# Performance work log

Measured on AMD Instinct MI355X. Metric: run time of the kernel, lower is better.

Reference implementation:

```python
import jax, jax.numpy as jnp
import numpy as np

EPS = 1e-5

def _ln(x, g, b):
    m = jnp.mean(x, axis=-1, keepdims=True)
    v = jnp.var(x, axis=-1, keepdims=True)
    return (x - m) / jnp.sqrt(v + EPS) * g + b

def _partition(x, nw):
    b, h, w, c = x.shape
    x = x.reshape(b, nw, h // nw, nw, w // nw, c).transpose(0, 1, 3, 2, 4, 5)
    return x.reshape(b * nw * nw, h // nw, w // nw, c)

def _merge(x, nw):
    b_, h, w, c = x.shape
    b = b_ // (nw * nw)
    x = x.reshape(b, nw, nw, h, w, c).transpose(0, 1, 3, 2, 4, 5)
    return x.reshape(b, nw * h, nw * w, c)

def _window_attn(q, k, v, width, height, nw, mask):
    b, _, c = q.shape
    q = q.reshape(b, height, width, c)
    k = k.reshape(b, height, width, c)
    v = v.reshape(b, height, width, c)
    sh, sw = (height // nw) // 2, (width // nw) // 2
    q = jnp.roll(q, (-sh, -sw), (1, 2))
    k = jnp.roll(k, (-sh, -sw), (1, 2))
    v = jnp.roll(v, (-sh, -sw), (1, 2))
    q = _partition(q, nw); k = _partition(k, nw); v = _partition(v, nw)
    N = (height // nw) * (width // nw)
    b_ = b * nw * nw
    qf = q.reshape(b_, N, c); kf = k.reshape(b_, N, c); vf = v.reshape(b_, N, c)
    scale = jnp.asarray(c, qf.dtype) ** 0.5
    scores = jnp.einsum('bnc,bmc->bnm', qf, kf) / scale  # [b_, N, N]
    scores = (scores.reshape(b, nw * nw, N, N) + mask[None]).reshape(b_, N, N)
    attn = jax.nn.softmax(scores, axis=-1)
    out = jnp.einsum('bnm,bmc->bnc', attn, vf)
    out = _merge(out.reshape(b_, height // nw, width // nw, c), nw)
    out = jnp.roll(out, (sh, sw), (1, 2))
    return out.reshape(b, height * width, c)

def _block(feat0, feat1, width, height, mask, nw, wq, wk, wv, wfc, g, be, ffn=None):
    q = feat0 @ wq; k = feat1 @ wk; v = feat1 @ wv
    a = _window_attn(q, k, v, width, height, nw, mask)
    a = _ln(a @ wfc, g, be)
    if ffn is not None:
        w1, w2, fg, fb = ffn
        h = jax.nn.gelu(jnp.concatenate([feat0, a], axis=-1) @ w1, approximate=False)
        a = _ln(h @ w2, fg, fb)
    return feat0 + a

def setup_inputs() -> dict:
    key = jax.random.key(0)
    B, H, W, NW, D = 8, 128, 128, 8, 256
    N = (H // NW) * (W // NW)
    ks = jax.random.split(key, 16)
    s = D ** -0.5
    return {
        'feat0': jax.random.normal(ks[0], (B, H * W, D), jnp.float32),
        'feat1': jax.random.normal(ks[1], (B, H * W, D), jnp.float32),
        'mask_attn': jax.random.normal(ks[2], (NW * NW, N, N), jnp.float32),
        'width': W, 'height': H, 'n_window': NW,
        'intra_wq': jax.random.normal(ks[3], (D, D), jnp.float32) * s,
        'intra_wk': jax.random.normal(ks[4], (D, D), jnp.float32) * s,
        'intra_wv': jax.random.normal(ks[5], (D, D), jnp.float32) * s,
        'intra_wfc': jax.random.normal(ks[6], (D, D), jnp.float32) * s,
        'intra_g': jnp.ones((D,), jnp.float32),
        'intra_b': jnp.zeros((D,), jnp.float32),
        'inter_wq': jax.random.normal(ks[7], (D, D), jnp.float32) * s,
        'inter_wk': jax.random.normal(ks[8], (D, D), jnp.float32) * s,
        'inter_wv': jax.random.normal(ks[9], (D, D), jnp.float32) * s,
        'inter_wfc': jax.random.normal(ks[10], (D, D), jnp.float32) * s,
        'inter_g': jnp.ones((D,), jnp.float32),
        'inter_b': jnp.zeros((D,), jnp.float32),
        'inter_w1': jax.random.normal(ks[11], (2 * D, 2 * D * 4), jnp.float32) * (2 * D) ** -0.5,
        'inter_w2': jax.random.normal(ks[12], (2 * D * 4, D), jnp.float32) * (2 * D * 4) ** -0.5,
        'inter_fg': jnp.ones((D,), jnp.float32),
        'inter_fb': jnp.zeros((D,), jnp.float32),
    }

def reference(feat0, feat1, mask_attn, width, height, n_window,
              intra_wq, intra_wk, intra_wv, intra_wfc, intra_g, intra_b,
              inter_wq, inter_wk, inter_wv, inter_wfc, inter_g, inter_b,
              inter_w1, inter_w2, inter_fg, inter_fb):
    f0 = _block(feat0, feat0, width, height, mask_attn, n_window,
                intra_wq, intra_wk, intra_wv, intra_wfc, intra_g, intra_b)
    out = _block(f0, feat1, width, height, mask_attn, n_window,
                 inter_wq, inter_wk, inter_wv, inter_wfc, inter_g, inter_b,
                 ffn=(inter_w1, inter_w2, inter_fg, inter_fb))
    return out
```

## Files before the change

### kernel.cpp

```cpp
#include <hip/hip_runtime.h>

typedef unsigned short u16;
typedef unsigned int   u32;

using f32x4  = __attribute__((ext_vector_type(4))) float;
using bf16x8 = __attribute__((ext_vector_type(8))) __bf16;

__device__ inline u16 f2bf(float f) {
  return __builtin_bit_cast(u16, (__bf16)f);
}
__device__ inline float bf2f(u16 v) {
  u32 u = ((u32)v) << 16;
  return __builtin_bit_cast(float, u);
}
__device__ inline u32 pk_bf16(float a, float b) {
  u32 d;
  asm("v_cvt_pk_bf16_f32 %0, %1, %2" : "=v"(d) : "v"(a), "v"(b));
  return d;
}

__device__ inline void gl_lds16(const u16* g, u16* l) {
  __builtin_amdgcn_global_load_lds((const __attribute__((address_space(1))) void*)g,
                                   (__attribute__((address_space(3))) void*)l,
                                   16, 0, 0);
}

__device__ inline int perm_fwd(int m) {
  int b = m >> 14, rem = m & 16383;
  int h = rem >> 7, w = rem & 127;
  int hr = (h - 8) & 127, wr = (w - 8) & 127;
  int win = (b << 6) | ((hr >> 4) << 3) | (wr >> 4);
  return (win << 8) | ((hr & 15) << 4) | (wr & 15);
}
__device__ inline int perm_inv(int r) {
  int win = r >> 8, t = r & 255;
  int b = win >> 6, wy = (win >> 3) & 7, wx = win & 7;
  int h = (((wy << 4) | (t >> 4)) + 8) & 127;
  int w = (((wx << 4) | (t & 15)) + 8) & 127;
  return (b << 14) | (h << 7) | w;
}


enum { MODE_QKV = 0, MODE_PV = 2, MODE_FFN1 = 4 };

template<int MODE>
__global__ __launch_bounds__(256)
void gemm_nt(const u16* __restrict__ A, int lda, long long sAz,
             const u16* __restrict__ Bt, int ldb, long long sBz,
             u16* __restrict__ OutB, float* __restrict__ OutF,
             const float* __restrict__ mask, int K, int ldo)
{
  __shared__ __align__(16) u16 sA[128 * 64];
  __shared__ __align__(16) u16 sB[128 * 64];

  const int tid  = threadIdx.x;
  const int lane = tid & 63;
  const int wave = tid >> 6;
  const int l15  = lane & 15;
  const int quad = lane >> 4;
  const int wm   = (wave >> 1) << 6;
  const int wn   = (wave & 1) << 6;
  const int z    = blockIdx.z;
  const int m0   = (int)(blockIdx.y) << 7;
  const int n0   = (int)(blockIdx.x) << 7;

  const u16* Ab = A  + (long long)z * sAz;
  const u16* Bb = Bt + (long long)z * sBz;

  const int cd = ((lane & 7) ^ ((lane >> 3) & 7)) << 3;
  const int rs = (wave << 5) + (lane >> 3);
  const u16* ga0 = Ab + (long long)(m0 + rs) * lda + cd;
  const u16* gb0 = Bb + (long long)(n0 + rs) * ldb + cd;
  u16* la0 = &sA[wave << 11];
  u16* lb0 = &sB[wave << 11];

  const f32x4 zero = {0.f, 0.f, 0.f, 0.f};
  f32x4 acc[4][4];
#pragma unroll
  for (int i = 0; i < 4; ++i)
#pragma unroll
    for (int j = 0; j < 4; ++j) acc[i][j] = zero;

  for (int k0 = 0; k0 < K; k0 += 64) {
    __syncthreads();
#pragma unroll
    for (int p = 0; p < 4; ++p) {
      gl_lds16(ga0 + k0 + (p << 3) * lda, la0 + (p << 9));
      gl_lds16(gb0 + k0 + (p << 3) * ldb, lb0 + (p << 9));
    }
    __syncthreads();
#pragma unroll
    for (int kk = 0; kk < 2; ++kk) {
      const int sw = (((quad | (kk << 2)) ^ (l15 & 7)) << 3);
      bf16x8 af[4], bfr[4];
#pragma unroll
      for (int i = 0; i < 4; ++i) {
        af[i]  = *(const bf16x8*)(sA + ((wm + (i << 4) + l15) << 6) + sw);
        bfr[i] = *(const bf16x8*)(sB + ((wn + (i << 4) + l15) << 6) + sw);
      }
#pragma unroll
      for (int i = 0; i < 4; ++i)
#pragma unroll
        for (int j = 0; j < 4; ++j)
          acc[i][j] = __builtin_amdgcn_mfma_f32_16x16x32_bf16(af[i], bfr[j], acc[i][j], 0, 0, 0);
    }
  }

#pragma unroll
  for (int i = 0; i < 4; ++i) {
#pragma unroll
    for (int r = 0; r < 4; ++r) {
      int mg = m0 + wm + (i << 4) + (quad << 2) + r;
      if constexpr (MODE == MODE_QKV) {
        u16* orow = OutB + (long long)(n0 >> 8) * ldo + ((long long)perm_fwd(mg) << 8);
#pragma unroll
        for (int j = 0; j < 4; ++j) {
          int ng = n0 + wn + (j << 4) + l15;
          orow[ng & 255] = f2bf(acc[i][j][r]);
        }
      } else if constexpr (MODE == MODE_PV) {
        u16* orow = OutB + ((long long)perm_inv((z << 8) + mg) << 8);
#pragma unroll
        for (int j = 0; j < 4; ++j) {
          int ng = n0 + wn + (j << 4) + l15;
          orow[ng] = f2bf(acc[i][j][r]);
        }
      } else {
        float gv[4];
#pragma unroll
        for (int j = 0; j < 4; ++j) {
          float v = acc[i][j][r];
          float t = v * fmaf(v * v, -0.071354816f, -1.5957691216f);
          gv[j] = v * __builtin_amdgcn_rcpf(1.0f + __expf(t));
        }
        uint2 d;
        d.x = pk_bf16(gv[0], gv[1]);
        d.y = pk_bf16(gv[2], gv[3]);
        *(uint2*)(OutB + (long long)mg * ldo + n0 + wn + (l15 << 2)) = d;
      }
    }
  }
}

__global__ __launch_bounds__(256)
void gemm_vt(const u16* __restrict__ Wt,
             const u16* __restrict__ Feat,
             u16* __restrict__ Vt)
{
  __shared__ __align__(16) u16 sA[128 * 64];
  __shared__ __align__(16) u16 sB[128 * 64];

  const int tid  = threadIdx.x;
  const int lane = tid & 63;
  const int wave = tid >> 6;
  const int l15  = lane & 15;
  const int quad = lane >> 4;
  const int wm   = (wave >> 1) << 6;
  const int wn   = (wave & 1) << 6;
  const int z    = blockIdx.z;
  const int m0   = (int)(blockIdx.y) << 7;
  const int n0   = (int)(blockIdx.x) << 7;

  const int cd = ((lane & 7) ^ ((lane >> 3) & 7)) << 3;
  const int rs = (wave << 5) + (lane >> 3);
  const u16* ga0 = Wt + (long long)(m0 + rs) * 256 + cd;
  const u16* gb0 = Feat + (long long)perm_inv((z << 8) + n0 + rs)        * 256 + cd;
  const u16* gb1 = Feat + (long long)perm_inv((z << 8) + n0 + rs + 8)    * 256 + cd;
  const u16* gb2 = Feat + (long long)perm_inv((z << 8) + n0 + rs + 16)   * 256 + cd;
  const u16* gb3 = Feat + (long long)perm_inv((z << 8) + n0 + rs + 24)   * 256 + cd;
  u16* la0 = &sA[wave << 11];
  u16* lb0 = &sB[wave << 11];

  const f32x4 zero = {0.f, 0.f, 0.f, 0.f};
  f32x4 acc[4][4];
#pragma unroll
  for (int i = 0; i < 4; ++i)
#pragma unroll
    for (int j = 0; j < 4; ++j) acc[i][j] = zero;

  for (int k0 = 0; k0 < 256; k0 += 64) {
    __syncthreads();
#pragma unroll
    for (int p = 0; p < 4; ++p)
      gl_lds16(ga0 + k0 + (p << 3) * 256, la0 + (p << 9));
    gl_lds16(gb0 + k0, lb0);
    gl_lds16(gb1 + k0, lb0 + 512);
    gl_lds16(gb2 + k0, lb0 + 1024);
    gl_lds16(gb3 + k0, lb0 + 1536);
    __syncthreads();
#pragma unroll
    for (int kk = 0; kk < 2; ++kk) {
      const int sw = (((quad | (kk << 2)) ^ (l15 & 7)) << 3);
      bf16x8 af[4], bfr[4];
#pragma unroll
      for (int i = 0; i < 4; ++i) {
        af[i]  = *(const bf16x8*)(sA + ((wm + (i << 4) + l15) << 6) + sw);
        bfr[i] = *(const bf16x8*)(sB + ((wn + (i << 4) + l15) << 6) + sw);
      }
#pragma unroll
      for (int i = 0; i < 4; ++i)
#pragma unroll
        for (int j = 0; j < 4; ++j)
          acc[i][j] = __builtin_amdgcn_mfma_f32_16x16x32_bf16(af[i], bfr[j], acc[i][j], 0, 0, 0);
    }
  }

#pragma unroll
  for (int i = 0; i < 4; ++i) {
#pragma unroll
    for (int r = 0; r < 4; ++r) {
      const int mg = m0 + wm + (i << 4) + (quad << 2) + r;
      u16* orow = Vt + (((long long)z) << 16) + ((long long)mg << 8);
#pragma unroll
      for (int j = 0; j < 4; ++j) {
        int ng = n0 + wn + (j << 4) + l15;
        orow[ng] = f2bf(acc[i][j][r]);
      }
    }
  }
}

__global__ __launch_bounds__(256)
void scores_softmax(const u16* __restrict__ Q, const u16* __restrict__ Kw,
                    const float* __restrict__ mask, u16* __restrict__ SP)
{
  __shared__ __align__(16) u16 sA[128 * 64];
  __shared__ __align__(16) u16 sB[256 * 64];

  const int tid  = threadIdx.x;
  const int lane = tid & 63;
  const int wave = tid >> 6;
  const int l15  = lane & 15;
  const int quad = lane >> 4;

  const int mhalf = (int)blockIdx.x;
  const int z     = (int)blockIdx.y;
  const int m0    = mhalf << 7;

  const u16* Ab = Q  + ((long long)z << 16);
  const u16* Bb = Kw + ((long long)z << 16);

  const int cd  = ((lane & 7) ^ ((lane >> 3) & 7)) << 3;
  const int rsA = (wave << 5) + (lane >> 3);
  const int rsB = (wave << 6) + (lane >> 3);
  const u16* ga0 = Ab + (long long)(m0 + rsA) * 256 + cd;
  const u16* gb0 = Bb + (long long)rsB * 256 + cd;
  u16* la0 = &sA[wave << 11];
  u16* lb0 = &sB[wave << 12];

  const f32x4 zero = {0.f, 0.f, 0.f, 0.f};
  f32x4 acc[2][16];
#pragma unroll
  for (int i = 0; i < 2; ++i)
#pragma unroll
    for (int j = 0; j < 16; ++j) acc[i][j] = zero;

  for (int k0 = 0; k0 < 256; k0 += 64) {
    __syncthreads();
#pragma unroll
    for (int p = 0; p < 4; ++p)
      gl_lds16(ga0 + k0 + (p << 3) * 256, la0 + (p << 9));
#pragma unroll
    for (int p = 0; p < 8; ++p)
      gl_lds16(gb0 + k0 + (p << 3) * 256, lb0 + (p << 9));
    __syncthreads();
#pragma unroll
    for (int kk = 0; kk < 2; ++kk) {
      const int sw = (((quad | (kk << 2)) ^ (l15 & 7)) << 3);
      bf16x8 af0 = *(const bf16x8*)(sA + (((wave << 5) + l15) << 6) + sw);
      bf16x8 af1 = *(const bf16x8*)(sA + (((wave << 5) + 16 + l15) << 6) + sw);
#pragma unroll
      for (int j = 0; j < 16; ++j) {
        bf16x8 bf = *(const bf16x8*)(sB + (((j << 4) + l15) << 6) + sw);
        acc[0][j] = __builtin_amdgcn_mfma_f32_16x16x32_bf16(af0, bf, acc[0][j], 0, 0, 0);
        acc[1][j] = __builtin_amdgcn_mfma_f32_16x16x32_bf16(af1, bf, acc[1][j], 0, 0, 0);
      }
    }
  }

  const float* mbase = mask + (((long long)(z & 63)) << 16);
#pragma unroll
  for (int i = 0; i < 2; ++i) {
#pragma unroll
    for (int r = 0; r < 4; ++r) {
      const int mg = m0 + (wave << 5) + (i << 4) + (quad << 2) + r;
      const float* mrow = mbase + ((long long)mg << 8);
      float sv[16];
      float mx = -3.0e38f;
#pragma unroll
      for (int j = 0; j < 16; ++j) {
        sv[j] = acc[i][j][r] * 0.0625f + mrow[(j << 4) + l15];
        mx = fmaxf(mx, sv[j]);
      }
#pragma unroll
      for (int o = 1; o < 16; o <<= 1) mx = fmaxf(mx, __shfl_xor(mx, o));
      float sum = 0.f;
#pragma unroll
      for (int j = 0; j < 16; ++j) { sv[j] = __expf(sv[j] - mx); sum += sv[j]; }
#pragma unroll
      for (int o = 1; o < 16; o <<= 1) sum += __shfl_xor(sum, o);
      const float inv = 1.0f / sum;
      u16* orow = SP + (((long long)z) << 16) + ((long long)mg << 8);
#pragma unroll
      for (int j = 0; j < 16; ++j) orow[(j << 4) + l15] = f2bf(sv[j] * inv);
    }
  }
}

enum { LN_XCAT0 = 0, LN_XCAT1 = 1, LN_OUT = 2 };

template<int MODE>
__global__ __launch_bounds__(256)
void gemm_ln(const u16* __restrict__ A, int lda,
             const u16* __restrict__ Bt,
             const float* __restrict__ G, const float* __restrict__ Bias,
             const float* __restrict__ ResF, const u16* __restrict__ ResB,
             float* __restrict__ OutF, u16* __restrict__ OutB, int K)
{
  __shared__ __align__(16) u16 sA[64 * 64];
  __shared__ __align__(16) u16 sB[256 * 64];

  const int tid  = threadIdx.x;
  const int lane = tid & 63;
  const int wave = tid >> 6;
  const int l15  = lane & 15;
  const int quad = lane >> 4;
  const int m0   = (int)blockIdx.x << 6;

  const int cd  = ((lane & 7) ^ ((lane >> 3) & 7)) << 3;
  const int rsA = (wave << 4) + (lane >> 3);
  const int rsB = (wave << 6) + (lane >> 3);
  const u16* ga0 = A  + (long long)(m0 + rsA) * lda + cd;
  const u16* gb0 = Bt + (long long)rsB * K + cd;
  u16* la0 = &sA[wave << 10];
  u16* lb0 = &sB[wave << 12];

  const f32x4 zero = {0.f, 0.f, 0.f, 0.f};
  f32x4 acc[16];
#pragma unroll
  for (int j = 0; j < 16; ++j) acc[j] = zero;

  for (int k0 = 0; k0 < K; k0 += 64) {
    __syncthreads();
#pragma unroll
    for (int p = 0; p < 2; ++p)
      gl_lds16(ga0 + k0 + (p << 3) * lda, la0 + (p << 9));
#pragma unroll
    for (int p = 0; p < 8; ++p)
      gl_lds16(gb0 + k0 + (p << 3) * K, lb0 + (p << 9));
    __syncthreads();
#pragma unroll
    for (int kk = 0; kk < 2; ++kk) {
      const int sw = (((quad | (kk << 2)) ^ (l15 & 7)) << 3);
      bf16x8 af = *(const bf16x8*)(sA + (((wave << 4) + l15) << 6) + sw);
#pragma unroll
      for (int j = 0; j < 16; ++j) {
        bf16x8 bf = *(const bf16x8*)(sB + (((j << 4) + l15) << 6) + sw);
        acc[j] = __builtin_amdgcn_mfma_f32_16x16x32_bf16(af, bf, acc[j], 0, 0, 0);
      }
    }
  }

  float gj[16], bj[16];
#pragma unroll
  for (int j = 0; j < 16; ++j) {
    gj[j] = G[(j << 4) + l15];
    bj[j] = Bias[(j << 4) + l15];
  }

#pragma unroll
  for (int r = 0; r < 4; ++r) {
    const int mg = m0 + (wave << 4) + (quad << 2) + r;
    float s = 0.f, s2 = 0.f;
#pragma unroll
    for (int j = 0; j < 16; ++j) {
      float v = acc[j][r];
      s += v; s2 += v * v;
    }
#pragma unroll
    for (int o = 1; o < 16; o <<= 1) { s += __shfl_xor(s, o); s2 += __shfl_xor(s2, o); }
    const float mean = s * (1.0f / 256.0f);
    const float var  = s2 * (1.0f / 256.0f) - mean * mean;
    const float rstd = rsqrtf(var + 1e-5f);
    if constexpr (MODE == LN_XCAT0) {
      u16* orow = OutB + ((long long)mg << 9);
      const float* rrow = ResF + ((long long)mg << 8);
#pragma unroll
      for (int j = 0; j < 16; ++j) {
        float v = (acc[j][r] - mean) * rstd * gj[j] + bj[j];
        orow[(j << 4) + l15] = f2bf(v + rrow[(j << 4) + l15]);
      }
    } else if constexpr (MODE == LN_XCAT1) {
      u16* orow = OutB + ((long long)mg << 9) + 256;
#pragma unroll
      for (int j = 0; j < 16; ++j) {
        float v = (acc[j][r] - mean) * rstd * gj[j] + bj[j];
        orow[(j << 4) + l15] = f2bf(v);
      }
    } else {
      const u16* rrow = ResB + ((long long)mg << 9);
      float* orow = OutF + ((long long)mg << 8);
#pragma unroll
      for (int j = 0; j < 16; ++j) {
        float v = (acc[j][r] - mean) * rstd * gj[j] + bj[j];
        orow[(j << 4) + l15] = v + bf2f(rrow[(j << 4) + l15]);
      }
    }
  }
}

__global__ __launch_bounds__(256)
void cvt_f32_bf16(const float* __restrict__ src, u16* __restrict__ dst, int n4)
{
  int i = blockIdx.x * 256 + threadIdx.x;
  if (i >= n4) return;
  float4 v = ((const float4*)src)[i];
  ushort4 u; u.x = f2bf(v.x); u.y = f2bf(v.y); u.z = f2bf(v.z); u.w = f2bf(v.w);
  ((ushort4*)dst)[i] = u;
}

__global__ __launch_bounds__(256)
void wtrans(const float* __restrict__ src, u16* __restrict__ dst, int R, int C)
{
  int idx = blockIdx.x * 256 + threadIdx.x;
  if (idx >= R * C) return;
  int r = idx / C, c = idx - r * C;
  dst[c * R + r] = f2bf(src[idx]);
}

__global__ __launch_bounds__(256)
void wtrans_w2(const float* __restrict__ src, u16* __restrict__ dst)
{
  int idx = blockIdx.x * 256 + threadIdx.x;
  int c = idx >> 11, q = idx & 2047;
  int f = (q & ~63) | ((q & 3) << 4) | ((q >> 2) & 15);
  dst[idx] = f2bf(src[f * 256 + c]);
}

extern "C" void kernel_launch(void* const* d_in, const int* in_sizes, int n_in,
                              void* d_out, int out_size, void* d_ws, size_t ws_size,
                              hipStream_t stream)
{
  (void)in_sizes; (void)n_in; (void)out_size;
  const float* feat0 = (const float*)d_in[0];
  const float* feat1 = (const float*)d_in[1];
  const float* mask  = (const float*)d_in[2];
  const float* wq1 = (const float*)d_in[6];
  const float* wk1 = (const float*)d_in[7];
  const float* wv1 = (const float*)d_in[8];
  const float* wf1 = (const float*)d_in[9];
  const float* g1  = (const float*)d_in[10];
  const float* b1  = (const float*)d_in[11];
  const float* wq2 = (const float*)d_in[12];
  const float* wk2 = (const float*)d_in[13];
  const float* wv2 = (const float*)d_in[14];
  const float* wf2 = (const float*)d_in[15];
  const float* g2  = (const float*)d_in[16];
  const float* b2  = (const float*)d_in[17];
  const float* w1  = (const float*)d_in[18];
  const float* w2  = (const float*)d_in[19];
  const float* fg  = (const float*)d_in[20];
  const float* fb  = (const float*)d_in[21];

  const size_t Mi = 1048576;
  const size_t WB = 4 * Mi;
  const int Mtot = 131072;

  int nc = 8;
  for (int c = 1; c <= 8; c <<= 1) {
    size_t S = (size_t)(Mtot / c) * 512;
    if (7 * S + WB <= ws_size) { nc = c; break; }
  }
  const int Mc = Mtot / nc;
  const size_t S = (size_t)Mc * 512;

  char* ws = (char*)d_ws;
  u16*   featb = (u16*)(ws);
  u16*   SPb   = featb;
  u16*   qw    = (u16*)(ws + S);
  u16*   Ob    = qw;
  u16*   hbuf  = featb;
  u16*   kw    = (u16*)(ws + 2 * S);
  u16*   vt    = (u16*)(ws + 4 * S);
  u16*   xcat  = (u16*)(ws + 5 * S);
  u16*   wb    = (u16*)(ws + 7 * S);
  u16* wq1t = wb;            u16* wk1t = wb + 65536;  u16* wv1t = wb + 131072; u16* wf1t = wb + 196608;
  u16* wq2t = wb + 262144;   u16* wk2t = wb + 327680; u16* wv2t = wb + 393216; u16* wf2t = wb + 458752;
  u16* w1t  = wb + 524288;
  u16* w2t  = wb + 524288 + 1048576;

  const dim3 blk(256);
  const dim3 gBig(2, Mc / 128, 1);
  const dim3 gQK(4, Mc / 128, 1);
  const int  Wc = Mc / 256;
  const dim3 gWin(2, 2, Wc);
  const dim3 gSS(2, Wc);
  const int  gRows = Mc / 4;
  const int  gLN   = Mc / 64;
  const int  MF = Mc / 2;
  const dim3 gF1(16, MF / 128, 1);
  const int  gLNF  = MF / 64;

  wtrans<<<256, blk, 0, stream>>>(wq1, wq1t, 256, 256);
  wtrans<<<256, blk, 0, stream>>>(wk1, wk1t, 256, 256);
  wtrans<<<256, blk, 0, stream>>>(wv1, wv1t, 256, 256);
  wtrans<<<256, blk, 0, stream>>>(wf1, wf1t, 256, 256);
  wtrans<<<256, blk, 0, stream>>>(wq2, wq2t, 256, 256);
  wtrans<<<256, blk, 0, stream>>>(wk2, wk2t, 256, 256);
  wtrans<<<256, blk, 0, stream>>>(wv2, wv2t, 256, 256);
  wtrans<<<256, blk, 0, stream>>>(wf2, wf2t, 256, 256);
  wtrans<<<4096, blk, 0, stream>>>(w1, w1t, 512, 2048);
  wtrans_w2<<<2048, blk, 0, stream>>>(w2, w2t);

  const int qkStride = Mc * 256;

  for (int c = 0; c < nc; ++c) {
    const long long off = (long long)c * Mc * 256;
    const float* f0in = feat0 + off;
    const float* f1in = feat1 + off;
    float* outp = (float*)d_out + off;

    cvt_f32_bf16<<<gRows, blk, 0, stream>>>(f0in, featb, Mc * 64);
    gemm_nt<MODE_QKV><<<gQK, blk, 0, stream>>>(featb, 256, 0, wq1t, 256, 0, qw, nullptr, nullptr, 256, qkStride);
    gemm_vt<<<gWin, blk, 0, stream>>>(wv1t, featb, vt);
    scores_softmax<<<gSS, blk, 0, stream>>>(qw, kw, mask, SPb);
    gemm_nt<MODE_PV><<<gWin, blk, 0, stream>>>(SPb, 256, 65536, vt, 256, 65536, Ob, nullptr, nullptr, 256, 0);
    gemm_ln<LN_XCAT0><<<gLN, blk, 0, stream>>>(Ob, 256, wf1t, g1, b1, f0in, nullptr, nullptr, xcat, 256);

    cvt_f32_bf16<<<gRows, blk, 0, stream>>>(f1in, featb, Mc * 64);
    gemm_nt<MODE_QKV><<<gBig, blk, 0, stream>>>(xcat, 512, 0, wq2t, 256, 0, qw, nullptr, nullptr, 512, 0);
    gemm_nt<MODE_QKV><<<gBig, blk, 0, stream>>>(featb, 256, 0, wk2t, 256, 0, kw, nullptr, nullptr, 256, 0);
    gemm_vt<<<gWin, blk, 0, stream>>>(wv2t, featb, vt);
    scores_softmax<<<gSS, blk, 0, stream>>>(qw, kw, mask, SPb);
    gemm_nt<MODE_PV><<<gWin, blk, 0, stream>>>(SPb, 256, 65536, vt, 256, 65536, Ob, nullptr, nullptr, 256, 0);
    gemm_ln<LN_XCAT1><<<gLN, blk, 0, stream>>>(Ob, 256, wf2t, g2, b2, nullptr, nullptr, nullptr, xcat, 256);

    for (int mc = 0; mc < 2; ++mc) {
      const u16* xc = xcat + (long long)mc * MF * 512;
      gemm_nt<MODE_FFN1><<<gF1, blk, 0, stream>>>(xc, 512, 0, w1t, 512, 0,
                                                  hbuf, nullptr, nullptr, 512, 2048);
      gemm_ln<LN_OUT><<<gLNF, blk, 0, stream>>>(hbuf, 2048, w2t, fg, fb, nullptr,
                                                xcat + (long long)mc * MF * 512,
                                                outp + (long long)mc * MF * 256, nullptr, 2048);
    }
  }
}
```

Baseline: 1.664 ms.

## Double-buffer LDS tiles with K=32 steps to overlap global loads with MFMA

All four GEMM-style kernels move from a single 64-wide K tile to two 32-wide LDS buffers. The next tile is prefetched via global_load_lds while MFMAs run on the current one, and each iteration needs one barrier instead of two. The LDS swizzle and row mapping are reworked for the 32-element row width. In exchange the loop has twice as many iterations, and the prefetch relies on the end-of-loop barrier to make the async LDS writes visible. That barrier may not wait for the outstanding global-load-to-LDS traffic unless the compiler inserts a vmcnt wait.

```diff
diff --git a/kernel.cpp b/kernel.cpp
--- a/kernel.cpp
+++ b/kernel.cpp
@@ -50,8 +50,8 @@
              u16* __restrict__ OutB, float* __restrict__ OutF,
              const float* __restrict__ mask, int K, int ldo)
 {
-  __shared__ __align__(16) u16 sA[128 * 64];
-  __shared__ __align__(16) u16 sB[128 * 64];
+  __shared__ __align__(16) u16 sA[2][128 * 32];
+  __shared__ __align__(16) u16 sB[2][128 * 32];
 
   const int tid  = threadIdx.x;
   const int lane = tid & 63;
@@ -67,12 +67,15 @@
   const u16* Ab = A  + (long long)z * sAz;
   const u16* Bb = Bt + (long long)z * sBz;
 
-  const int cd = ((lane & 7) ^ ((lane >> 3) & 7)) << 3;
-  const int rs = (wave << 5) + (lane >> 3);
+  const int cd = ((lane & 3) ^ ((lane >> 3) & 3)) << 3;
+  const int rs = (wave << 5) + (lane >> 2);
   const u16* ga0 = Ab + (long long)(m0 + rs) * lda + cd;
+  const u16* ga1 = ga0 + 16ll * lda;
   const u16* gb0 = Bb + (long long)(n0 + rs) * ldb + cd;
-  u16* la0 = &sA[wave << 11];
-  u16* lb0 = &sB[wave << 11];
+  const u16* gb1 = gb0 + 16ll * ldb;
+  const int lofs = wave << 10;
+
+  const int sw = ((((l15 >> 1) & 3) ^ quad) << 3);
 
   const f32x4 zero = {0.f, 0.f, 0.f, 0.f};
   f32x4 acc[4][4];
@@ -81,29 +84,34 @@
 #pragma unroll
     for (int j = 0; j < 4; ++j) acc[i][j] = zero;
 
-  for (int k0 = 0; k0 < K; k0 += 64) {
+  gl_lds16(ga0, &sA[0][lofs]);
+  gl_lds16(ga1, &sA[0][lofs] + 512);
+  gl_lds16(gb0, &sB[0][lofs]);
+  gl_lds16(gb1, &sB[0][lofs] + 512);
+  __syncthreads();
+
+  int cur = 0;
+  for (int k0 = 0; k0 < K; k0 += 32) {
+    if (k0 + 32 < K) {
+      const int nxt = cur ^ 1;
+      gl_lds16(ga0 + k0 + 32, &sA[nxt][lofs]);
+      gl_lds16(ga1 + k0 + 32, &sA[nxt][lofs] + 512);
+      gl_lds16(gb0 + k0 + 32, &sB[nxt][lofs]);
+      gl_lds16(gb1 + k0 + 32, &sB[nxt][lofs] + 512);
+    }
+    bf16x8 af[4], bfr[4];
+#pragma unroll
+    for (int i = 0; i < 4; ++i) {
+      af[i]  = *(const bf16x8*)(&sA[cur][0] + ((wm + (i << 4) + l15) << 5) + sw);
+      bfr[i] = *(const bf16x8*)(&sB[cur][0] + ((wn + (i << 4) + l15) << 5) + sw);
+    }
+#pragma unroll
+    for (int i = 0; i < 4; ++i)
+#pragma unroll
+      for (int j = 0; j < 4; ++j)
+        acc[i][j] = __builtin_amdgcn_mfma_f32_16x16x32_bf16(af[i], bfr[j], acc[i][j], 0, 0, 0);
     __syncthreads();
-#pragma unroll
-    for (int p = 0; p < 4; ++p) {
-      gl_lds16(ga0 + k0 + (p << 3) * lda, la0 + (p << 9));
-      gl_lds16(gb0 + k0 + (p << 3) * ldb, lb0 + (p << 9));
-    }
-    __syncthreads();
-#pragma unroll
-    for (int kk = 0; kk < 2; ++kk) {
-      const int sw = (((quad | (kk << 2)) ^ (l15 & 7)) << 3);
-      bf16x8 af[4], bfr[4];
-#pragma unroll
-      for (int i = 0; i < 4; ++i) {
-        af[i]  = *(const bf16x8*)(sA + ((wm + (i << 4) + l15) << 6) + sw);
-        bfr[i] = *(const bf16x8*)(sB + ((wn + (i << 4) + l15) << 6) + sw);
-      }
-#pragma unroll
-      for (int i = 0; i < 4; ++i)
-#pragma unroll
-        for (int j = 0; j < 4; ++j)
-          acc[i][j] = __builtin_amdgcn_mfma_f32_16x16x32_bf16(af[i], bfr[j], acc[i][j], 0, 0, 0);
-    }
+    cur ^= 1;
   }
 
 #pragma unroll
@@ -147,8 +155,8 @@
              const u16* __restrict__ Feat,
              u16* __restrict__ Vt)
 {
-  __shared__ __align__(16) u16 sA[128 * 64];
-  __shared__ __align__(16) u16 sB[128 * 64];
+  __shared__ __align__(16) u16 sA[2][128 * 32];
+  __shared__ __align__(16) u16 sB[2][128 * 32];
 
   const int tid  = threadIdx.x;
   const int lane = tid & 63;
@@ -161,15 +169,15 @@
   const int m0   = (int)(blockIdx.y) << 7;
   const int n0   = (int)(blockIdx.x) << 7;
 
-  const int cd = ((lane & 7) ^ ((lane >> 3) & 7)) << 3;
-  const int rs = (wave << 5) + (lane >> 3);
+  const int cd = ((lane & 3) ^ ((lane >> 3) & 3)) << 3;
+  const int rs = (wave << 5) + (lane >> 2);
   const u16* ga0 = Wt + (long long)(m0 + rs) * 256 + cd;
-  const u16* gb0 = Feat + (long long)perm_inv((z << 8) + n0 + rs)        * 256 + cd;
-  const u16* gb1 = Feat + (long long)perm_inv((z << 8) + n0 + rs + 8)    * 256 + cd;
-  const u16* gb2 = Feat + (long long)perm_inv((z << 8) + n0 + rs + 16)   * 256 + cd;
-  const u16* gb3 = Feat + (long long)perm_inv((z << 8) + n0 + rs + 24)   * 256 + cd;
-  u16* la0 = &sA[wave << 11];
-  u16* lb0 = &sB[wave << 11];
+  const u16* ga1 = ga0 + 16ll * 256;
+  const u16* gb0 = Feat + (long long)perm_inv((z << 8) + n0 + rs)      * 256 + cd;
+  const u16* gb1 = Feat + (long long)perm_inv((z << 8) + n0 + rs + 16) * 256 + cd;
+  const int lofs = wave << 10;
+
+  const int sw = ((((l15 >> 1) & 3) ^ quad) << 3);
 
   const f32x4 zero = {0.f, 0.f, 0.f, 0.f};
   f32x4 acc[4][4];
@@ -178,31 +186,34 @@
 #pragma unroll
     for (int j = 0; j < 4; ++j) acc[i][j] = zero;
 
-  for (int k0 = 0; k0 < 256; k0 += 64) {
+  gl_lds16(ga0, &sA[0][lofs]);
+  gl_lds16(ga1, &sA[0][lofs] + 512);
+  gl_lds16(gb0, &sB[0][lofs]);
+  gl_lds16(gb1, &sB[0][lofs] + 512);
+  __syncthreads();
+
+  int cur = 0;
+  for (int k0 = 0; k0 < 256; k0 += 32) {
+    if (k0 + 32 < 256) {
+      const int nxt = cur ^ 1;
+      gl_lds16(ga0 + k0 + 32, &sA[nxt][lofs]);
+      gl_lds16(ga1 + k0 + 32, &sA[nxt][lofs] + 512);
+      gl_lds16(gb0 + k0 + 32, &sB[nxt][lofs]);
+      gl_lds16(gb1 + k0 + 32, &sB[nxt][lofs] + 512);
+    }
+    bf16x8 af[4], bfr[4];
+#pragma unroll
+    for (int i = 0; i < 4; ++i) {
+      af[i]  = *(const bf16x8*)(&sA[cur][0] + ((wm + (i << 4) + l15) << 5) + sw);
+      bfr[i] = *(const bf16x8*)(&sB[cur][0] + ((wn + (i << 4) + l15) << 5) + sw);
+    }
+#pragma unroll
+    for (int i = 0; i < 4; ++i)
+#pragma unroll
+      for (int j = 0; j < 4; ++j)
+        acc[i][j] = __builtin_amdgcn_mfma_f32_16x16x32_bf16(af[i], bfr[j], acc[i][j], 0, 0, 0);
     __syncthreads();
-#pragma unroll
-    for (int p = 0; p < 4; ++p)
-      gl_lds16(ga0 + k0 + (p << 3) * 256, la0 + (p << 9));
-    gl_lds16(gb0 + k0, lb0);
-    gl_lds16(gb1 + k0, lb0 + 512);
-    gl_lds16(gb2 + k0, lb0 + 1024);
-    gl_lds16(gb3 + k0, lb0 + 1536);
-    __syncthreads();
-#pragma unroll
-    for (int kk = 0; kk < 2; ++kk) {
-      const int sw = (((quad | (kk << 2)) ^ (l15 & 7)) << 3);
-      bf16x8 af[4], bfr[4];
-#pragma unroll
-      for (int i = 0; i < 4; ++i) {
-        af[i]  = *(const bf16x8*)(sA + ((wm + (i << 4) + l15) << 6) + sw);
-        bfr[i] = *(const bf16x8*)(sB + ((wn + (i << 4) + l15) << 6) + sw);
-      }
-#pragma unroll
-      for (int i = 0; i < 4; ++i)
-#pragma unroll
-        for (int j = 0; j < 4; ++j)
-          acc[i][j] = __builtin_amdgcn_mfma_f32_16x16x32_bf16(af[i], bfr[j], acc[i][j], 0, 0, 0);
-    }
+    cur ^= 1;
   }
 
 #pragma unroll
@@ -224,8 +235,8 @@
 void scores_softmax(const u16* __restrict__ Q, const u16* __restrict__ Kw,
                     const float* __restrict__ mask, u16* __restrict__ SP)
 {
-  __shared__ __align__(16) u16 sA[128 * 64];
-  __shared__ __align__(16) u16 sB[256 * 64];
+  __shared__ __align__(16) u16 sA[2][128 * 32];
+  __shared__ __align__(16) u16 sB[2][256 * 32];
 
   const int tid  = threadIdx.x;
   const int lane = tid & 63;
@@ -240,13 +251,16 @@
   const u16* Ab = Q  + ((long long)z << 16);
   const u16* Bb = Kw + ((long long)z << 16);
 
-  const int cd  = ((lane & 7) ^ ((lane >> 3) & 7)) << 3;
-  const int rsA = (wave << 5) + (lane >> 3);
-  const int rsB = (wave << 6) + (lane >> 3);
+  const int cd  = ((lane & 3) ^ ((lane >> 3) & 3)) << 3;
+  const int rsA = (wave << 5) + (lane >> 2);
+  const int rsB = (wave << 6) + (lane >> 2);
   const u16* ga0 = Ab + (long long)(m0 + rsA) * 256 + cd;
+  const u16* ga1 = ga0 + 16ll * 256;
   const u16* gb0 = Bb + (long long)rsB * 256 + cd;
-  u16* la0 = &sA[wave << 11];
-  u16* lb0 = &sB[wave << 12];
+  const int lofsA = wave << 10;
+  const int lofsB = wave << 11;
+
+  const int sw = ((((l15 >> 1) & 3) ^ quad) << 3);
 
   const f32x4 zero = {0.f, 0.f, 0.f, 0.f};
   f32x4 acc[2][16];
@@ -255,27 +269,33 @@
 #pragma unroll
     for (int j = 0; j < 16; ++j) acc[i][j] = zero;
 
-  for (int k0 = 0; k0 < 256; k0 += 64) {
+  gl_lds16(ga0, &sA[0][lofsA]);
+  gl_lds16(ga1, &sA[0][lofsA] + 512);
+#pragma unroll
+  for (int p = 0; p < 4; ++p)
+    gl_lds16(gb0 + (p << 4) * 256, &sB[0][lofsB] + (p << 9));
+  __syncthreads();
+
+  int cur = 0;
+  for (int k0 = 0; k0 < 256; k0 += 32) {
+    if (k0 + 32 < 256) {
+      const int nxt = cur ^ 1;
+      gl_lds16(ga0 + k0 + 32, &sA[nxt][lofsA]);
+      gl_lds16(ga1 + k0 + 32, &sA[nxt][lofsA] + 512);
+#pragma unroll
+      for (int p = 0; p < 4; ++p)
+        gl_lds16(gb0 + k0 + 32 + (p << 4) * 256, &sB[nxt][lofsB] + (p << 9));
+    }
+    bf16x8 af0 = *(const bf16x8*)(&sA[cur][0] + (((wave << 5) + l15) << 5) + sw);
+    bf16x8 af1 = *(const bf16x8*)(&sA[cur][0] + (((wave << 5) + 16 + l15) << 5) + sw);
+#pragma unroll
+    for (int j = 0; j < 16; ++j) {
+      bf16x8 bf = *(const bf16x8*)(&sB[cur][0] + (((j << 4) + l15) << 5) + sw);
+      acc[0][j] = __builtin_amdgcn_mfma_f32_16x16x32_bf16(af0, bf, acc[0][j], 0, 0, 0);
+      acc[1][j] = __builtin_amdgcn_mfma_f32_16x16x32_bf16(af1, bf, acc[1][j], 0, 0, 0);
+    }
     __syncthreads();
-#pragma unroll
-    for (int p = 0; p < 4; ++p)
-      gl_lds16(ga0 + k0 + (p << 3) * 256, la0 + (p << 9));
-#pragma unroll
-    for (int p = 0; p < 8; ++p)
-      gl_lds16(gb0 + k0 + (p << 3) * 256, lb0 + (p << 9));
-    __syncthreads();
-#pragma unroll
-    for (int kk = 0; kk < 2; ++kk) {
-      const int sw = (((quad | (kk << 2)) ^ (l15 & 7)) << 3);
-      bf16x8 af0 = *(const bf16x8*)(sA + (((wave << 5) + l15) << 6) + sw);
-      bf16x8 af1 = *(const bf16x8*)(sA + (((wave << 5) + 16 + l15) << 6) + sw);
-#pragma unroll
-      for (int j = 0; j < 16; ++j) {
-        bf16x8 bf = *(const bf16x8*)(sB + (((j << 4) + l15) << 6) + sw);
-        acc[0][j] = __builtin_amdgcn_mfma_f32_16x16x32_bf16(af0, bf, acc[0][j], 0, 0, 0);
-        acc[1][j] = __builtin_amdgcn_mfma_f32_16x16x32_bf16(af1, bf, acc[1][j], 0, 0, 0);
-      }
-    }
+    cur ^= 1;
   }
 
   const float* mbase = mask + (((long long)(z & 63)) << 16);
@@ -317,8 +337,8 @@
              const float* __restrict__ ResF, const u16* __restrict__ ResB,
              float* __restrict__ OutF, u16* __restrict__ OutB, int K)
 {
-  __shared__ __align__(16) u16 sA[64 * 64];
-  __shared__ __align__(16) u16 sB[256 * 64];
+  __shared__ __align__(16) u16 sA[2][64 * 32];
+  __shared__ __align__(16) u16 sB[2][256 * 32];
 
   const int tid  = threadIdx.x;
   const int lane = tid & 63;
@@ -327,38 +347,44 @@
   const int quad = lane >> 4;
   const int m0   = (int)blockIdx.x << 6;
 
-  const int cd  = ((lane & 7) ^ ((lane >> 3) & 7)) << 3;
-  const int rsA = (wave << 4) + (lane >> 3);
-  const int rsB = (wave << 6) + (lane >> 3);
+  const int cd  = ((lane & 3) ^ ((lane >> 3) & 3)) << 3;
+  const int rsA = (wave << 4) + (lane >> 2);
+  const int rsB = (wave << 6) + (lane >> 2);
   const u16* ga0 = A  + (long long)(m0 + rsA) * lda + cd;
   const u16* gb0 = Bt + (long long)rsB * K + cd;
-  u16* la0 = &sA[wave << 10];
-  u16* lb0 = &sB[wave << 12];
+  const int lofsA = wave << 9;
+  const int lofsB = wave << 11;
+
+  const int sw = ((((l15 >> 1) & 3) ^ quad) << 3);
 
   const f32x4 zero = {0.f, 0.f, 0.f, 0.f};
   f32x4 acc[16];
 #pragma unroll
   for (int j = 0; j < 16; ++j) acc[j] = zero;
 
-  for (int k0 = 0; k0 < K; k0 += 64) {
+  gl_lds16(ga0, &sA[0][lofsA]);
+#pragma unroll
+  for (int p = 0; p < 4; ++p)
+    gl_lds16(gb0 + (long long)(p << 4) * K, &sB[0][lofsB] + (p << 9));
+  __syncthreads();
+
+  int cur = 0;
+  for (int k0 = 0; k0 < K; k0 += 32) {
+    if (k0 + 32 < K) {
+      const int nxt = cur ^ 1;
+      gl_lds16(ga0 + k0 + 32, &sA[nxt][lofsA]);
+#pragma unroll
+      for (int p = 0; p < 4; ++p)
+        gl_lds16(gb0 + k0 + 32 + (long long)(p << 4) * K, &sB[nxt][lofsB] + (p << 9));
+    }
+    bf16x8 af = *(const bf16x8*)(&sA[cur][0] + (((wave << 4) + l15) << 5) + sw);
+#pragma unroll
+    for (int j = 0; j < 16; ++j) {
+      bf16x8 bf = *(const bf16x8*)(&sB[cur][0] + (((j << 4) + l15) << 5) + sw);
+      acc[j] = __builtin_amdgcn_mfma_f32_16x16x32_bf16(af, bf, acc[j], 0, 0, 0);
+    }
     __syncthreads();
-#pragma unroll
-    for (int p = 0; p < 2; ++p)
-      gl_lds16(ga0 + k0 + (p << 3) * lda, la0 + (p << 9));
-#pragma unroll
-    for (int p = 0; p < 8; ++p)
-      gl_lds16(gb0 + k0 + (p << 3) * K, lb0 + (p << 9));
-    __syncthreads();
-#pragma unroll
-    for (int kk = 0; kk < 2; ++kk) {
-      const int sw = (((quad | (kk << 2)) ^ (l15 & 7)) << 3);
-      bf16x8 af = *(const bf16x8*)(sA + (((wave << 4) + l15) << 6) + sw);
-#pragma unroll
-      for (int j = 0; j < 16; ++j) {
-        bf16x8 bf = *(const bf16x8*)(sB + (((j << 4) + l15) << 6) + sw);
-        acc[j] = __builtin_amdgcn_mfma_f32_16x16x32_bf16(af, bf, acc[j], 0, 0, 0);
-      }
-    }
+    cur ^= 1;
   }
 
   float gj[16], bj[16];
```

Result: slower. 1.837 ms (+10.4%).
